# Performance work log

Measured on AMD Instinct MI355X. Metric: run time of the kernel, lower is better.

Reference implementation:

```python
import jax, jax.numpy as jnp
import numpy as np

E = 256; H = 8; HD = E // H
L_LEN = 300; A_LEN = 250
T = 768; B = 4
NEG = -1e9


def setup_inputs() -> dict:
    rng = jax.random.key(0)
    ks = jax.random.split(rng, 16)
    n = lambda k, s, sc=1.0: jax.random.normal(k, s, dtype=jnp.float32) * sc
    return {
        "query": n(ks[0], (T, B, E)),
        "key": n(ks[1], (T, B, E)),
        "value": n(ks[2], (T, B, E)),
        "in_proj_w": n(ks[3], (3 * E, E), 0.05),
        "in_proj_b": jnp.zeros((3 * E,), jnp.float32),
        "out_w": n(ks[4], (7, E, E), 0.05),
        "out_b": jnp.zeros((7, E), jnp.float32),
        "s_l_w": n(ks[5], (E, 4 * E), 0.05),
        "s_l_b": jnp.zeros((E,), jnp.float32),
        "s_a_w": n(ks[6], (E, 4 * E), 0.05),
        "s_a_b": jnp.zeros((E,), jnp.float32),
        "s_v_w": n(ks[7], (E, 4 * E), 0.05),
        "s_v_b": jnp.zeros((E,), jnp.float32),
        "final_w": n(ks[8], (E, E), 0.05),
        "final_b": jnp.zeros((E,), jnp.float32),
    }


def _forward(query, key, value, in_proj_w, in_proj_b, out_w, out_b,
             s_l_w, s_l_b, s_a_w, s_a_b, s_v_w, s_v_b, final_w, final_b):
    t, b, e = query.shape
    scaling = HD ** -0.5
    Wq, Wk, Wv = in_proj_w[:E], in_proj_w[E:2 * E], in_proj_w[2 * E:]
    bq, bk, bv = in_proj_b[:E], in_proj_b[E:2 * E], in_proj_b[2 * E:]
    q = (query @ Wq.T + bq) * scaling
    k = key @ Wk.T + bk
    v = value @ Wv.T + bv
    # (T, B, E) -> (B*H, T, HD)
    sh = lambda x: x.reshape(t, b * H, HD).transpose(1, 0, 2)
    q, k, v = sh(q), sh(k), sh(v)
    # shared QK^T, reused by all 7 masked branches
    scores = jnp.einsum('bth,bsh->bts', q, k)  # (B*H, T, T)
    idx = jnp.arange(t)
    seg = jnp.where(idx < L_LEN, 0, jnp.where(idx < L_LEN + A_LEN, 1, 2))

    def branch(i, mods):
        # m[j] = 1 iff position j belongs to one of the selected modalities
        m = sum((seg == s) for s in mods).astype(scores.dtype)  # (T,)
        # additive mask: in-set query attends only in-set keys; out-of-set
        # query rows get all -1e9 (uniform softmax, zeroed by row mask below)
        add = jnp.where((m[:, None] * m[None, :]) > 0, 0.0, NEG)
        w = jax.nn.softmax(scores + add, axis=-1) * m[None, :, None]
        o = jnp.einsum('bts,bsh->bth', w, v * m[None, :, None])
        o = o.transpose(1, 0, 2).reshape(t, b, e)
        return o @ out_w[i].T + out_b[i]

    attn_lav = branch(0, (0, 1, 2))
    attn_la = branch(1, (0, 1))
    attn_lv = branch(2, (0, 2))
    attn_av = branch(3, (1, 2))
    attn_l = branch(4, (0,))
    attn_a = branch(5, (1,))
    attn_v = branch(6, (2,))

    sl = jnp.concatenate([attn_lav, attn_la, attn_lv, attn_l], -1) @ s_l_w.T + s_l_b
    sa = jnp.concatenate([attn_lav, attn_la, attn_av, attn_a], -1) @ s_a_w.T + s_a_b
    sv = jnp.concatenate([attn_lav, attn_lv, attn_av, attn_v], -1) @ s_v_w.T + s_v_b
    return (sl + sa + sv) @ final_w.T + final_b


def reference(query, key, value, in_proj_w, in_proj_b, out_w, out_b,
              s_l_w, s_l_b, s_a_w, s_a_b, s_v_w, s_v_b, final_w, final_b):
    return _forward(query, key, value, in_proj_w, in_proj_b, out_w, out_b,
                    s_l_w, s_l_b, s_a_w, s_a_b, s_v_w, s_v_b, final_w, final_b)
```

## Files before the change

### kernel.cpp

```cpp
#include <hip/hip_runtime.h>
#include <hip/hip_bf16.h>

#define E 256
#define H 8
#define HD 32
#define T 768
#define B 4
#define BH 32

typedef __attribute__((ext_vector_type(8))) short bf16x8;
typedef __attribute__((ext_vector_type(4))) float f32x4;
typedef __attribute__((ext_vector_type(16))) float f32x16;

__device__ __forceinline__ float b2f(__hip_bfloat16 x) { return __bfloat162float(x); }

__device__ __forceinline__ unsigned short f2bf_u(float x) {
    __hip_bfloat16 h = __float2bfloat16(x);
    return *(unsigned short*)&h;
}
__device__ __forceinline__ float bfu2f(unsigned short u) {
    return __uint_as_float(((unsigned int)u) << 16);
}

__device__ __forceinline__ int detect_f32(const void* query) {
    const unsigned short* q = (const unsigned short*)query;
    int lane = threadIdx.x & 63;
    int bad = 0;
    #pragma unroll
    for (int i = 0; i < 4; ++i) {
        float v = bfu2f(q[lane + i * 64]);
        bad |= (!(v == v) || fabsf(v) > 1e4f) ? 1 : 0;
    }
    return __any(bad) ? 1 : 0;
}

__device__ __forceinline__ void f8_split(const float* v, bf16x8& h, bf16x8& l) {
    #pragma unroll
    for (int e = 0; e < 8; ++e) {
        unsigned short hu = f2bf_u(v[e]);
        h[e] = (short)hu;
        l[e] = (short)f2bf_u(v[e] - bfu2f(hu));
    }
}

#define MFMA3(ACC, AH, AL, BH_, BL_)                                         \
    ACC = __builtin_amdgcn_mfma_f32_16x16x32_bf16(AH, BH_, ACC, 0, 0, 0);    \
    ACC = __builtin_amdgcn_mfma_f32_16x16x32_bf16(AH, BL_, ACC, 0, 0, 0);    \
    ACC = __builtin_amdgcn_mfma_f32_16x16x32_bf16(AL, BH_, ACC, 0, 0, 0);

#define MFMA3W(ACC, AH, AL, BH_, BL_)                                        \
    ACC = __builtin_amdgcn_mfma_f32_32x32x16_bf16(AH, BH_, ACC, 0, 0, 0);    \
    ACC = __builtin_amdgcn_mfma_f32_32x32x16_bf16(AH, BL_, ACC, 0, 0, 0);    \
    ACC = __builtin_amdgcn_mfma_f32_32x32x16_bf16(AL, BH_, ACC, 0, 0, 0);

__device__ __forceinline__ bf16x8 mk8(int a, int b, int c, int d) {
    union { int i[4]; bf16x8 v; } u;
    u.i[0] = a; u.i[1] = b; u.i[2] = c; u.i[3] = d;
    return u.v;
}

__device__ __forceinline__ float ldu(const void* p, size_t i, int f32) {
    if (f32) return ((const float*)p)[i];
    return b2f(((const __hip_bfloat16*)p)[i]);
}

__device__ __forceinline__ float gsum_load(int i, int r2, int r,
                                           const void* sl, const void* sa,
                                           const void* sv, int f32)
{
    size_t base = (size_t)r2 * 1024;
    switch (i) {
        case 0: return ldu(sl, base + r, f32) + ldu(sa, base + r, f32) + ldu(sv, base + r, f32);
        case 1: return ldu(sl, base + 256 + r, f32) + ldu(sa, base + 256 + r, f32);
        case 2: return ldu(sl, base + 512 + r, f32) + ldu(sv, base + 256 + r, f32);
        case 3: return ldu(sa, base + 512 + r, f32) + ldu(sv, base + 512 + r, f32);
        case 4: return ldu(sl, base + 768 + r, f32);
        case 5: return ldu(sa, base + 768 + r, f32);
        default: return ldu(sv, base + 768 + r, f32);
    }
}

__global__ __launch_bounds__(256) void conv_kernel(
    const void* query, const void* key, const void* value, const void* w,
    const void* sl, const void* sa, const void* sv, const void* outw,
    unsigned short* __restrict__ XFh, unsigned short* __restrict__ XFl,
    unsigned short* __restrict__ WFh, unsigned short* __restrict__ WFl,
    unsigned short* __restrict__ GFh, unsigned short* __restrict__ GFl,
    unsigned short* __restrict__ OWFh, unsigned short* __restrict__ OWFl)
{
    int f32 = detect_f32(query);
    int item = blockIdx.x * 256 + threadIdx.x;
    if (item < 294912) {
        int inp = item / 98304;
        int rem = item % 98304;
        int row = rem >> 5, kg = rem & 31;
        const void* X = (inp == 0) ? query : (inp == 1) ? key : value;
        float v[8];
        if (f32) {
            const float4* p = (const float4*)((const float*)X +
                               (size_t)row * 256 + kg * 8);
            *(float4*)&v[0] = p[0];
            *(float4*)&v[4] = p[1];
        } else {
            #pragma unroll
            for (int j = 0; j < 8; ++j)
                v[j] = ldu(X, (size_t)row * 256 + kg * 8 + j, 0);
        }
        bf16x8 h, l;
        f8_split(v, h, l);
        int rb = row >> 4, kb = kg >> 2;
        int lane = (row & 15) | ((kg & 3) << 4);
        size_t idx = (((size_t)(inp * 192 + rb) * 8 + kb) * 64 + lane) * 8;
        *(bf16x8*)&XFh[idx] = h;
        *(bf16x8*)&XFl[idx] = l;
    } else if (item < 319488) {
        int rem = item - 294912;
        int gc = rem >> 5, kg = rem & 31;
        float v[8];
        if (f32) {
            const float4* p = (const float4*)((const float*)w +
                               (size_t)gc * 256 + kg * 8);
            *(float4*)&v[0] = p[0];
            *(float4*)&v[4] = p[1];
        } else {
            #pragma unroll
            for (int j = 0; j < 8; ++j)
                v[j] = ldu(w, (size_t)gc * 256 + kg * 8 + j, 0);
        }
        bf16x8 h, l;
        f8_split(v, h, l);
        int sec = gc >> 8, c = gc & 255;
        int cb = c >> 4, kb = kg >> 2;
        int lane = (c & 15) | ((kg & 3) << 4);
        size_t idx = (((size_t)(sec * 16 + cb) * 8 + kb) * 64 + lane) * 8;
        *(bf16x8*)&WFh[idx] = h;
        *(bf16x8*)&WFl[idx] = l;
    } else if (item < 376832) {
        int rem = item - 319488;
        int i = rem >> 13;
        int rest = rem & 8191;
        int r2 = rest >> 5, kg = rest & 31;
        float v[8];
        #pragma unroll
        for (int j = 0; j < 8; ++j)
            v[j] = gsum_load(i, r2, kg * 8 + j, sl, sa, sv, f32);
        bf16x8 h, l;
        f8_split(v, h, l);
        int rb = r2 >> 4, kb = kg >> 2;
        int lane = (r2 & 15) | ((kg & 3) << 4);
        size_t idx = (((size_t)(i * 16 + rb) * 8 + kb) * 64 + lane) * 8;
        *(bf16x8*)&GFh[idx] = h;
        *(bf16x8*)&GFl[idx] = l;
    } else if (item < 434176) {
        int rem = item - 376832;
        int i = rem >> 13;
        int rest = rem & 8191;
        int kg = rest >> 8, c = rest & 255;
        float v[8];
        #pragma unroll
        for (int j = 0; j < 8; ++j)
            v[j] = ldu(outw, (size_t)i * 65536 + (kg * 8 + j) * 256 + c, f32);
        bf16x8 h, l;
        f8_split(v, h, l);
        int cb = c >> 4, kb = kg >> 2;
        int lane = (c & 15) | ((kg & 3) << 4);
        size_t idx = (((size_t)(i * 16 + cb) * 8 + kb) * 64 + lane) * 8;
        *(bf16x8*)&OWFh[idx] = h;
        *(bf16x8*)&OWFl[idx] = l;
    }
}

__global__ __launch_bounds__(256) void qkv_mfma_kernel(
    const unsigned short* __restrict__ XFh, const unsigned short* __restrict__ XFl,
    const unsigned short* __restrict__ WFh, const unsigned short* __restrict__ WFl,
    const void* bias, const void* query,
    float* __restrict__ qws,
    unsigned short* __restrict__ KRh, unsigned short* __restrict__ KRl,
    unsigned short* __restrict__ VFh, unsigned short* __restrict__ VFl)
{
    int f32 = detect_f32(query);
    int bx = blockIdx.x;
    int rb = blockIdx.y;
    int sec = bx >> 2, cg = bx & 3;
    int w = threadIdx.x >> 6, lane = threadIdx.x & 63;
    int m = lane & 15, quad = lane >> 4;
    int cb = cg * 4 + w;

    const unsigned short* Ah = XFh + (((size_t)(sec * 192 + rb) * 8) * 64 + lane) * 8;
    const unsigned short* Al = XFl + (((size_t)(sec * 192 + rb) * 8) * 64 + lane) * 8;
    const unsigned short* Bh = WFh + (((size_t)(sec * 16 + cb) * 8) * 64 + lane) * 8;
    const unsigned short* Bl = WFl + (((size_t)(sec * 16 + cb) * 8) * 64 + lane) * 8;

    f32x4 acc = {};
    #pragma unroll
    for (int kb = 0; kb < 8; ++kb) {
        size_t off = (size_t)kb * 512;
        bf16x8 ah = *(const bf16x8*)(Ah + off);
        bf16x8 al = *(const bf16x8*)(Al + off);
        bf16x8 bh = *(const bf16x8*)(Bh + off);
        bf16x8 bl = *(const bf16x8*)(Bl + off);
        MFMA3(acc, ah, al, bh, bl)
    }

    int c_local = cb * 16 + m;
    float bv = ldu(bias, sec * 256 + c_local, f32);
    int h = c_local >> 5, hd = c_local & 31;

    if (sec == 0) {
        #pragma unroll
        for (int rr = 0; rr < 4; ++rr) {
            int row = rb * 16 + quad * 4 + rr;
            int t = row >> 2, b = row & 3;
            float val = (acc[rr] + bv) * 0.17677669529663687f;
            qws[((size_t)((b * H + h) * T + t)) * HD + hd] = val;
        }
    } else if (sec == 1) {
        #pragma unroll
        for (int rr = 0; rr < 4; ++rr) {
            int row = rb * 16 + quad * 4 + rr;
            int s = row >> 2, b = row & 3;
            int bh_ = b * 8 + h;
            float val = acc[rr] + bv;
            unsigned short hu = f2bf_u(val);
            unsigned short lu = f2bf_u(val - bfu2f(hu));
            size_t bi = ((size_t)bh_ * 768 + s) * 32 + hd;
            KRh[bi] = hu;
            KRl[bi] = lu;
        }
    } else {
        #pragma unroll
        for (int rr = 0; rr < 4; ++rr) {
            int row = rb * 16 + quad * 4 + rr;
            int s = row >> 2, b = row & 3;
            int bh_ = b * 8 + h;
            float val = acc[rr] + bv;
            unsigned short hu = f2bf_u(val);
            unsigned short lu = f2bf_u(val - bfu2f(hu));
            int s16 = s >> 4, hp = (s >> 3) & 1, j = s & 7;
            size_t bi = (((size_t)bh_ * 48 + s16) * 64 + hp * 32 + hd) * 8 + j;
            VFh[bi] = hu;
            VFl[bi] = lu;
        }
    }
}

__global__ __launch_bounds__(256) void wcomb1_mfma_kernel(
    const unsigned short* __restrict__ GFh, const unsigned short* __restrict__ GFl,
    const unsigned short* __restrict__ OWFh, const unsigned short* __restrict__ OWFl,
    float* __restrict__ Mtmp)
{
    int cgrp = blockIdx.x;
    int rb   = blockIdx.y;
    int i    = blockIdx.z;
    int w = threadIdx.x >> 6, lane = threadIdx.x & 63;
    int m = lane & 15, quad = lane >> 4;
    int cb = cgrp * 4 + w;

    const unsigned short* Ah = GFh + (((size_t)(i * 16 + rb) * 8) * 64 + lane) * 8;
    const unsigned short* Al = GFl + (((size_t)(i * 16 + rb) * 8) * 64 + lane) * 8;
    const unsigned short* Bh = OWFh + (((size_t)(i * 16 + cb) * 8) * 64 + lane) * 8;
    const unsigned short* Bl = OWFl + (((size_t)(i * 16 + cb) * 8) * 64 + lane) * 8;

    f32x4 acc = {};
    #pragma unroll
    for (int kb = 0; kb < 8; ++kb) {
        size_t off = (size_t)kb * 512;
        bf16x8 ah = *(const bf16x8*)(Ah + off);
        bf16x8 al = *(const bf16x8*)(Al + off);
        bf16x8 bh = *(const bf16x8*)(Bh + off);
        bf16x8 bl = *(const bf16x8*)(Bl + off);
        MFMA3(acc, ah, al, bh, bl)
    }
    #pragma unroll
    for (int rr = 0; rr < 4; ++rr) {
        int r2 = rb * 16 + quad * 4 + rr;
        Mtmp[(size_t)i * 65536 + r2 * 256 + cb * 16 + m] = acc[rr];
    }
}

__global__ __launch_bounds__(256, 3) void attn_mfma_kernel(
    const float* __restrict__ qws,
    const unsigned short* __restrict__ KRh, const unsigned short* __restrict__ KRl,
    const unsigned short* __restrict__ VFh, const unsigned short* __restrict__ VFl,
    unsigned short* __restrict__ Ohi, unsigned short* __restrict__ Olo)
{
    int tile = blockIdx.x;
    int bh   = blockIdx.y;
    int t0 = tile * 32;
    int tid = threadIdx.x;
    int w = tid >> 6, lane = tid & 63;
    int ln = lane & 31, h = lane >> 5;

    __shared__ float AC2[2][3][32][36];
    __shared__ float SS2[2][3][32];

    bf16x8 qbh[2], qbl[2];
    {
        const float* qr = qws + ((size_t)bh * T + t0 + ln) * HD + h * 8;
        #pragma unroll
        for (int c = 0; c < 2; ++c) {
            float qv[8];
            *(float4*)&qv[0] = *(const float4*)(qr + c * 16);
            *(float4*)&qv[4] = *(const float4*)(qr + c * 16 + 4);
            f8_split(qv, qbh[c], qbl[c]);
        }
    }

    f32x16 accA = {}, accB = {};
    float ssA = 0.f, ssB = 0.f;

    for (int q = 0; q < 3; ++q) {
        int ch = w * 3 + q;
        int sbase = ch * 64;
        int route = (ch == 5) ? 1 : (ch == 4 || ch == 8) ? 2 : 0;
        int bnd = (ch == 4) ? 300 : 550;
        bool c12 = (ch == 4);

        int PH[2][8], PL[2][8];
        #pragma unroll
        for (int st = 0; st < 2; ++st) {
            size_t krow = ((size_t)bh * 768 + sbase + st * 32 + ln) * 32 + h * 8;
            bf16x8 kh0 = *(const bf16x8*)(KRh + krow);
            bf16x8 kl0 = *(const bf16x8*)(KRl + krow);
            bf16x8 kh1 = *(const bf16x8*)(KRh + krow + 16);
            bf16x8 kl1 = *(const bf16x8*)(KRl + krow + 16);
            f32x16 d = {};
            MFMA3W(d, kh0, kl0, qbh[0], qbl[0])
            MFMA3W(d, kh1, kl1, qbh[1], qbl[1])

            int EH[16], EL[16];
            #pragma unroll
            for (int r = 0; r < 16; ++r) {
                float e = __expf(d[r]);
                if (route == 2) {
                    int s = sbase + st * 32 + (r & 3) + 8 * (r >> 2) + 4 * h;
                    if (s < bnd) ssA += e; else ssB += e;
                } else if (route == 1) ssB += e;
                else ssA += e;
                unsigned int eb = __float_as_uint(e);
                float lo = e - __uint_as_float(eb & 0xffff0000u);
                EH[r] = (int)eb;
                EL[r] = (int)__float_as_uint(lo);
            }
            #pragma unroll
            for (int p = 0; p < 8; ++p) {
                PH[st][p] = (int)(((unsigned)EH[2*p] >> 16) |
                                  ((unsigned)EH[2*p+1] & 0xffff0000u));
                PL[st][p] = (int)(((unsigned)EL[2*p] >> 16) |
                                  ((unsigned)EL[2*p+1] & 0xffff0000u));
            }
        }

        #pragma unroll
        for (int ks = 0; ks < 4; ++ks) {
            int st = ks >> 1, cc = 4 * (ks & 1);
            size_t vidx = (((size_t)bh * 48 + ch * 4 + ks) * 64 + lane) * 8;
            bf16x8 vbh = *(const bf16x8*)(VFh + vidx);
            bf16x8 vbl = *(const bf16x8*)(VFl + vidx);

            int sh0 = __shfl_xor(PH[st][cc+0], 32);
            int sh1 = __shfl_xor(PH[st][cc+1], 32);
            int sh2 = __shfl_xor(PH[st][cc+2], 32);
            int sh3 = __shfl_xor(PH[st][cc+3], 32);
            int sl0 = __shfl_xor(PL[st][cc+0], 32);
            int sl1 = __shfl_xor(PL[st][cc+1], 32);
            int sl2 = __shfl_xor(PL[st][cc+2], 32);
            int sl3 = __shfl_xor(PL[st][cc+3], 32);
            int FH0 = h ? sh2 : PH[st][cc+0];
            int FH1 = h ? sh3 : PH[st][cc+1];
            int FH2 = h ? PH[st][cc+2] : sh0;
            int FH3 = h ? PH[st][cc+3] : sh1;
            int FL0 = h ? sl2 : PL[st][cc+0];
            int FL1 = h ? sl3 : PL[st][cc+1];
            int FL2 = h ? PL[st][cc+2] : sl0;
            int FL3 = h ? PL[st][cc+3] : sl1;
            bf16x8 feh = mk8(FH0, FH1, FH2, FH3);
            bf16x8 fel = mk8(FL0, FL1, FL2, FL3);

            if (route == 0)      { MFMA3W(accA, feh, fel, vbh, vbl) }
            else if (route == 1) { MFMA3W(accB, feh, fel, vbh, vbl) }
            else {
                if (ks < 2)       { MFMA3W(accA, feh, fel, vbh, vbl) }
                else if (ks == 3) { MFMA3W(accB, feh, fel, vbh, vbl) }
                else {
                    int a0 = h ? (c12 ? FH0 : 0) : FH0;
                    int a1 = h ? (c12 ? FH1 : 0) : FH1;
                    int a2 = h ? 0 : FH2;
                    int a3 = h ? 0 : (c12 ? FH3 : 0);
                    int b0 = h ? (c12 ? 0 : FH0) : 0;
                    int b1 = h ? (c12 ? 0 : FH1) : 0;
                    int b2 = h ? FH2 : 0;
                    int b3 = h ? FH3 : (c12 ? 0 : FH3);
                    int la0 = h ? (c12 ? FL0 : 0) : FL0;
                    int la1 = h ? (c12 ? FL1 : 0) : FL1;
                    int la2 = h ? 0 : FL2;
                    int la3 = h ? 0 : (c12 ? FL3 : 0);
                    int lb0 = h ? (c12 ? 0 : FL0) : 0;
                    int lb1 = h ? (c12 ? 0 : FL1) : 0;
                    int lb2 = h ? FL2 : 0;
                    int lb3 = h ? FL3 : (c12 ? 0 : FL3);
                    bf16x8 fha = mk8(a0, a1, a2, a3), fla = mk8(la0, la1, la2, la3);
                    bf16x8 fhb = mk8(b0, b1, b2, b3), flb = mk8(lb0, lb1, lb2, lb3);
                    MFMA3W(accA, fha, fla, vbh, vbl)
                    MFMA3W(accB, fhb, flb, vbh, vbl)
                }
            }
        }
    }

    ssA += __shfl_xor(ssA, 32);
    ssB += __shfl_xor(ssB, 32);

    int bsel = w & 1;
    f32x16 zz = {};
    f32x16 o0 = (w <= 1) ? accA : zz;
    f32x16 o1 = (w == 1) ? accB : (w == 2) ? accA : zz;
    f32x16 o2 = (w == 2) ? accB : (w == 3) ? accA : zz;
    float s0 = (w <= 1) ? ssA : 0.f;
    float s1 = (w == 1) ? ssB : (w == 2) ? ssA : 0.f;
    float s2 = (w == 2) ? ssB : (w == 3) ? ssA : 0.f;

    if (w < 2) {
        #pragma unroll
        for (int r = 0; r < 16; ++r) {
            int t = (r & 3) + 8 * (r >> 2) + 4 * h;
            AC2[bsel][0][t][ln] = o0[r];
            AC2[bsel][1][t][ln] = o1[r];
            AC2[bsel][2][t][ln] = o2[r];
        }
        if (h == 0) {
            SS2[bsel][0][ln] = s0;
            SS2[bsel][1][ln] = s1;
            SS2[bsel][2][ln] = s2;
        }
    }
    __syncthreads();
    if (w >= 2) {
        #pragma unroll
        for (int r = 0; r < 16; ++r) {
            int t = (r & 3) + 8 * (r >> 2) + 4 * h;
            AC2[bsel][1][t][ln] += o1[r];
            AC2[bsel][2][t][ln] += o2[r];
        }
        if (h == 0) {
            SS2[bsel][1][ln] += s1;
            SS2[bsel][2][ln] += s2;
        }
    }
    __syncthreads();

    int tt = tid >> 3, q4 = tid & 7;
    float Pv[3][4], S[3];
    #pragma unroll
    for (int sg = 0; sg < 3; ++sg) {
        const float4 a = *(const float4*)&AC2[0][sg][tt][q4 * 4];
        const float4 b = *(const float4*)&AC2[1][sg][tt][q4 * 4];
        Pv[sg][0] = a.x + b.x; Pv[sg][1] = a.y + b.y;
        Pv[sg][2] = a.z + b.z; Pv[sg][3] = a.w + b.w;
        S[sg] = SS2[0][sg][tt] + SS2[1][sg][tt];
    }

    int t_glob = t0 + tt;
    int g = (t_glob < 300) ? 0 : (t_glob < 550 ? 1 : 2);
    int b_ = bh >> 3, h_ = bh & 7;
    int row = t_glob * B + b_;
    int lslot = (row & 15) + ((q4 >> 1) << 4);
    int j0 = (q4 & 1) * 4;
    size_t fbase = (((size_t)(row >> 4) * 56 + h_) * 64 + lslot) * 8 + j0;
    const int masks[7] = {7, 3, 5, 6, 1, 2, 4};
    #pragma unroll
    for (int i = 0; i < 7; ++i) {
        int mm = masks[i];
        float n0 = 0.f, n1 = 0.f, n2 = 0.f, n3 = 0.f, den = 0.f;
        if (mm & 1) { n0 += Pv[0][0]; n1 += Pv[0][1]; n2 += Pv[0][2]; n3 += Pv[0][3]; den += S[0]; }
        if (mm & 2) { n0 += Pv[1][0]; n1 += Pv[1][1]; n2 += Pv[1][2]; n3 += Pv[1][3]; den += S[1]; }
        if (mm & 4) { n0 += Pv[2][0]; n1 += Pv[2][1]; n2 += Pv[2][2]; n3 += Pv[2][3]; den += S[2]; }
        float r = 1.f / den;
        int live = (mm >> g) & 1;
        float o[4];
        o[0] = live ? n0 * r : 0.f;
        o[1] = live ? n1 * r : 0.f;
        o[2] = live ? n2 * r : 0.f;
        o[3] = live ? n3 * r : 0.f;
        ushort4 hi4, lo4;
        unsigned short* hp = (unsigned short*)&hi4;
        unsigned short* lp = (unsigned short*)&lo4;
        #pragma unroll
        for (int j = 0; j < 4; ++j) {
            unsigned short hu = f2bf_u(o[j]);
            hp[j] = hu;
            lp[j] = f2bf_u(o[j] - bfu2f(hu));
        }
        size_t addr = fbase + (size_t)i * (8 * 64 * 8);
        *(ushort4*)&Ohi[addr] = hi4;
        *(ushort4*)&Olo[addr] = lo4;
    }
}

__global__ __launch_bounds__(256) void wcomb2_gemm_kernel(
    const float* __restrict__ Mtmp, const void* finalw, const void* query,
    unsigned short* __restrict__ DThi, unsigned short* __restrict__ DTlo)
{
    int f32 = detect_f32(query);
    int bx = blockIdx.x;
    int by = blockIdx.y;
    int i  = blockIdx.z;
    int tid = threadIdx.x;
    int tx = tid & 15, ty = tid >> 4;
    int colbase = bx * 32, rowbase = by * 32;
    __shared__ __align__(16) float AsT[32][34];
    __shared__ __align__(16) float Bs[32][34];
    float acc[2][2] = {};

    for (int kb = 0; kb < 8; ++kb) {
        __syncthreads();
        #pragma unroll
        for (int l = 0; l < 4; ++l) {
            int idx = l * 256 + tid;
            int c = idx & 31, kk = idx >> 5;
            AsT[kk][c] = Mtmp[(size_t)i * 65536 + (kb * 32 + kk) * 256 + rowbase + c];
            int k2 = idx & 31, n = idx >> 5;
            Bs[k2][n] = ldu(finalw, (size_t)(colbase + n) * 256 + kb * 32 + k2, f32);
        }
        __syncthreads();
        #pragma unroll 8
        for (int kk = 0; kk < 32; ++kk) {
            const float2 av = *(const float2*)&AsT[kk][ty * 2];
            const float2 bv = *(const float2*)&Bs[kk][tx * 2];
            acc[0][0] += av.x * bv.x; acc[0][1] += av.x * bv.y;
            acc[1][0] += av.y * bv.x; acc[1][1] += av.y * bv.y;
        }
    }
    #pragma unroll
    for (int u = 0; u < 2; ++u)
        #pragma unroll
        for (int v = 0; v < 2; ++v) {
            int c = rowbase + ty * 2 + u, e = colbase + tx * 2 + v;
            float a = acc[u][v];
            unsigned short hu = f2bf_u(a);
            size_t fidx = (((size_t)(e >> 4) * 56 + i * 8 + (c >> 5)) * 64
                           + (e & 15) + (((c >> 3) & 3) << 4)) * 8 + (c & 7);
            DThi[fidx] = hu;
            DTlo[fidx] = f2bf_u(a - bfu2f(hu));
        }
}

__global__ __launch_bounds__(256) void bias1_kernel(
    const void* sl, const void* sa, const void* sv, const void* outb,
    const void* slb, const void* sab, const void* svb,
    const void* query, float* __restrict__ c0)
{
    int f32 = detect_f32(query);
    int r2 = blockIdx.x, m = threadIdx.x;
    __shared__ float red[256];
    float acc = 0.f;
    #pragma unroll
    for (int i = 0; i < 7; ++i)
        acc += ldu(outb, i * 256 + m, f32) * gsum_load(i, r2, m, sl, sa, sv, f32);
    red[m] = acc;
    __syncthreads();
    for (int s = 128; s > 0; s >>= 1) {
        if (m < s) red[m] += red[m + s];
        __syncthreads();
    }
    if (m == 0)
        c0[r2] = red[0] + ldu(slb, r2, f32) + ldu(sab, r2, f32) + ldu(svb, r2, f32);
}

__global__ __launch_bounds__(256) void bias2_kernel(
    const float* __restrict__ c0, const void* finalw, const void* finalb,
    const void* query, float* __restrict__ d0)
{
    int f32 = detect_f32(query);
    int e = blockIdx.x, r = threadIdx.x;
    __shared__ float red[256];
    red[r] = c0[r] * ldu(finalw, (size_t)e * 256 + r, f32);
    __syncthreads();
    for (int s = 128; s > 0; s >>= 1) {
        if (r < s) red[r] += red[r + s];
        __syncthreads();
    }
    if (r == 0)
        d0[e] = red[0] + ldu(finalb, e, f32);
}

__global__ __launch_bounds__(256) void final_gemm_mfma_kernel(
    const unsigned short* __restrict__ Ohi, const unsigned short* __restrict__ Olo,
    const unsigned short* __restrict__ DThi, const unsigned short* __restrict__ DTlo,
    const float* __restrict__ d0, const void* query,
    void* __restrict__ outv)
{
    int f32 = detect_f32(query);
    int bx = blockIdx.x;
    int by = blockIdx.y;
    int w  = threadIdx.x >> 6;
    int lane = threadIdx.x & 63;
    int m = lane & 15, quad = lane >> 4;
    int R0 = by * 16, C0 = bx * 64 + w * 16;

    int t0 = R0 >> 2, t1 = (R0 + 15) >> 2;
    int g0 = (t0 < 300) ? 0 : (t0 < 550 ? 1 : 2);
    int g1 = (t1 < 300) ? 0 : (t1 < 550 ? 1 : 2);
    int activeset = (1 << g0) | (1 << g1);
    const int masks[7] = {7, 3, 5, 6, 1, 2, 4};

    const unsigned short* Abase_h = Ohi + (size_t)by * 56 * 512 + lane * 8;
    const unsigned short* Abase_l = Olo + (size_t)by * 56 * 512 + lane * 8;
    const unsigned short* Bbase_h = DThi + (size_t)(bx * 4 + w) * 56 * 512 + lane * 8;
    const unsigned short* Bbase_l = DTlo + (size_t)(bx * 4 + w) * 56 * 512 + lane * 8;

    f32x4 acc = {};
    for (int i = 0; i < 7; ++i) {
        if (!(masks[i] & activeset)) continue;
        #pragma unroll
        for (int kb = 0; kb < 8; ++kb) {
            size_t off = (size_t)(i * 8 + kb) * 512;
            bf16x8 ah = *(const bf16x8*)(Abase_h + off);
            bf16x8 al = *(const bf16x8*)(Abase_l + off);
            bf16x8 bh = *(const bf16x8*)(Bbase_h + off);
            bf16x8 bl = *(const bf16x8*)(Bbase_l + off);
            acc = __builtin_amdgcn_mfma_f32_16x16x32_bf16(ah, bh, acc, 0, 0, 0);
            acc = __builtin_amdgcn_mfma_f32_16x16x32_bf16(ah, bl, acc, 0, 0, 0);
            acc = __builtin_amdgcn_mfma_f32_16x16x32_bf16(al, bh, acc, 0, 0, 0);
        }
    }
    float dv = d0[C0 + m];
    #pragma unroll
    for (int r = 0; r < 4; ++r) {
        int row = R0 + quad * 4 + r;
        int col = C0 + m;
        float val = acc[r] + dv;
        if (f32) ((float*)outv)[(size_t)row * 256 + col] = val;
        else ((__hip_bfloat16*)outv)[(size_t)row * 256 + col] = __float2bfloat16(val);
    }
}

extern "C" void kernel_launch(void* const* d_in, const int* in_sizes, int n_in,
                              void* d_out, int out_size, void* d_ws, size_t ws_size,
                              hipStream_t stream) {
    const void* query     = d_in[0];
    const void* key       = d_in[1];
    const void* value     = d_in[2];
    const void* in_proj_w = d_in[3];
    const void* in_proj_b = d_in[4];
    const void* out_w     = d_in[5];
    const void* out_b     = d_in[6];
    const void* s_l_w     = d_in[7];
    const void* s_l_b     = d_in[8];
    const void* s_a_w     = d_in[9];
    const void* s_a_b     = d_in[10];
    const void* s_v_w     = d_in[11];
    const void* s_v_b     = d_in[12];
    const void* final_w   = d_in[13];
    const void* final_b   = d_in[14];

    float* ws     = (float*)d_ws;
    float* qws    = ws;
    unsigned short* KRh = (unsigned short*)(ws + 786432);
    unsigned short* KRl = KRh + 786432;
    unsigned short* VFh = (unsigned short*)(ws + 1572864);
    unsigned short* VFl = VFh + 786432;
    unsigned short* Ohi = (unsigned short*)(ws + 2359296);
    unsigned short* Olo = (unsigned short*)(ws + 5111808);
    unsigned short* XFh = (unsigned short*)(ws + 2359296);
    unsigned short* XFl = XFh + 2359296;
    unsigned short* WFh = XFl + 2359296;
    unsigned short* WFl = WFh + 196608;
    unsigned short* GFh = (unsigned short*)(ws + 4915200);
    unsigned short* GFl = GFh + 458752;
    unsigned short* OWFh = GFl + 458752;
    unsigned short* OWFl = OWFh + 458752;
    float* Mtmp   = ws + 7864320;
    unsigned short* DThi = (unsigned short*)(ws + 8323072);
    unsigned short* DTlo = (unsigned short*)(ws + 8552448);
    float* d0     = ws + 8781824;
    float* c0     = Mtmp;

    conv_kernel<<<1696, 256, 0, stream>>>(query, key, value, in_proj_w,
                                          s_l_w, s_a_w, s_v_w, out_w,
                                          XFh, XFl, WFh, WFl,
                                          GFh, GFl, OWFh, OWFl);
    qkv_mfma_kernel<<<dim3(12, 192), 256, 0, stream>>>(XFh, XFl, WFh, WFl,
                                                       in_proj_b, query, qws,
                                                       KRh, KRl, VFh, VFl);
    wcomb1_mfma_kernel<<<dim3(4, 16, 7), 256, 0, stream>>>(GFh, GFl, OWFh, OWFl,
                                                           Mtmp);
    attn_mfma_kernel<<<dim3(24, 32), 256, 0, stream>>>(qws, KRh, KRl, VFh, VFl,
                                                       Ohi, Olo);
    wcomb2_gemm_kernel<<<dim3(8, 8, 7), 256, 0, stream>>>(Mtmp, final_w, query,
                                                          DThi, DTlo);
    bias1_kernel<<<256, 256, 0, stream>>>(s_l_w, s_a_w, s_v_w, out_b,
                                          s_l_b, s_a_b, s_v_b, query, c0);
    bias2_kernel<<<256, 256, 0, stream>>>(c0, final_w, final_b, query, d0);
    final_gemm_mfma_kernel<<<dim3(4, 192), 256, 0, stream>>>(Ohi, Olo, DThi, DTlo,
                                                             d0, query, d_out);
}
```

Measured before the change: 183.3 us.

## Merge independent kernels into three staged launches to cut launch count

Folds the eight kernel launches into four by packing independent work into shared grids. Bias1 joins the conversion kernel, QKV projection plus wcomb1 plus bias2 form one launch, and attention plus wcomb2 form another, with roles picked by block index ranges. This removes launch gaps and lets the smaller independent pieces fill idle CUs alongside the large ones. In exchange, merged kernels share the largest register and LDS footprint and the attention launch bounds. c0 moves to its own buffer so it no longer aliases Mtmp.

```diff
diff --git a/kernel.cpp b/kernel.cpp
--- a/kernel.cpp
+++ b/kernel.cpp
@@ -80,508 +80,503 @@
     }
 }
 
-__global__ __launch_bounds__(256) void conv_kernel(
+__global__ __launch_bounds__(256) void stage1_kernel(
     const void* query, const void* key, const void* value, const void* w,
     const void* sl, const void* sa, const void* sv, const void* outw,
+    const void* outb, const void* slb, const void* sab, const void* svb,
     unsigned short* __restrict__ XFh, unsigned short* __restrict__ XFl,
     unsigned short* __restrict__ WFh, unsigned short* __restrict__ WFl,
     unsigned short* __restrict__ GFh, unsigned short* __restrict__ GFl,
-    unsigned short* __restrict__ OWFh, unsigned short* __restrict__ OWFl)
+    unsigned short* __restrict__ OWFh, unsigned short* __restrict__ OWFl,
+    float* __restrict__ c0)
 {
+    __shared__ float red[256];
     int f32 = detect_f32(query);
-    int item = blockIdx.x * 256 + threadIdx.x;
-    if (item < 294912) {
-        int inp = item / 98304;
-        int rem = item % 98304;
-        int row = rem >> 5, kg = rem & 31;
-        const void* X = (inp == 0) ? query : (inp == 1) ? key : value;
-        float v[8];
-        if (f32) {
-            const float4* p = (const float4*)((const float*)X +
-                               (size_t)row * 256 + kg * 8);
-            *(float4*)&v[0] = p[0];
-            *(float4*)&v[4] = p[1];
-        } else {
+    if (blockIdx.x < 1696) {
+        int item = blockIdx.x * 256 + threadIdx.x;
+        if (item < 294912) {
+            int inp = item / 98304;
+            int rem = item % 98304;
+            int row = rem >> 5, kg = rem & 31;
+            const void* X = (inp == 0) ? query : (inp == 1) ? key : value;
+            float v[8];
+            if (f32) {
+                const float4* p = (const float4*)((const float*)X +
+                                   (size_t)row * 256 + kg * 8);
+                *(float4*)&v[0] = p[0];
+                *(float4*)&v[4] = p[1];
+            } else {
+                #pragma unroll
+                for (int j = 0; j < 8; ++j)
+                    v[j] = ldu(X, (size_t)row * 256 + kg * 8 + j, 0);
+            }
+            bf16x8 h, l;
+            f8_split(v, h, l);
+            int rb = row >> 4, kb = kg >> 2;
+            int lane = (row & 15) | ((kg & 3) << 4);
+            size_t idx = (((size_t)(inp * 192 + rb) * 8 + kb) * 64 + lane) * 8;
+            *(bf16x8*)&XFh[idx] = h;
+            *(bf16x8*)&XFl[idx] = l;
+        } else if (item < 319488) {
+            int rem = item - 294912;
+            int gc = rem >> 5, kg = rem & 31;
+            float v[8];
+            if (f32) {
+                const float4* p = (const float4*)((const float*)w +
+                                   (size_t)gc * 256 + kg * 8);
+                *(float4*)&v[0] = p[0];
+                *(float4*)&v[4] = p[1];
+            } else {
+                #pragma unroll
+                for (int j = 0; j < 8; ++j)
+                    v[j] = ldu(w, (size_t)gc * 256 + kg * 8 + j, 0);
+            }
+            bf16x8 h, l;
+            f8_split(v, h, l);
+            int sec = gc >> 8, c = gc & 255;
+            int cb = c >> 4, kb = kg >> 2;
+            int lane = (c & 15) | ((kg & 3) << 4);
+            size_t idx = (((size_t)(sec * 16 + cb) * 8 + kb) * 64 + lane) * 8;
+            *(bf16x8*)&WFh[idx] = h;
+            *(bf16x8*)&WFl[idx] = l;
+        } else if (item < 376832) {
+            int rem = item - 319488;
+            int i = rem >> 13;
+            int rest = rem & 8191;
+            int r2 = rest >> 5, kg = rest & 31;
+            float v[8];
             #pragma unroll
             for (int j = 0; j < 8; ++j)
-                v[j] = ldu(X, (size_t)row * 256 + kg * 8 + j, 0);
-        }
-        bf16x8 h, l;
-        f8_split(v, h, l);
-        int rb = row >> 4, kb = kg >> 2;
-        int lane = (row & 15) | ((kg & 3) << 4);
-        size_t idx = (((size_t)(inp * 192 + rb) * 8 + kb) * 64 + lane) * 8;
-        *(bf16x8*)&XFh[idx] = h;
-        *(bf16x8*)&XFl[idx] = l;
-    } else if (item < 319488) {
-        int rem = item - 294912;
-        int gc = rem >> 5, kg = rem & 31;
-        float v[8];
-        if (f32) {
-            const float4* p = (const float4*)((const float*)w +
-                               (size_t)gc * 256 + kg * 8);
-            *(float4*)&v[0] = p[0];
-            *(float4*)&v[4] = p[1];
-        } else {
+                v[j] = gsum_load(i, r2, kg * 8 + j, sl, sa, sv, f32);
+            bf16x8 h, l;
+            f8_split(v, h, l);
+            int rb = r2 >> 4, kb = kg >> 2;
+            int lane = (r2 & 15) | ((kg & 3) << 4);
+            size_t idx = (((size_t)(i * 16 + rb) * 8 + kb) * 64 + lane) * 8;
+            *(bf16x8*)&GFh[idx] = h;
+            *(bf16x8*)&GFl[idx] = l;
+        } else if (item < 434176) {
+            int rem = item - 376832;
+            int i = rem >> 13;
+            int rest = rem & 8191;
+            int kg = rest >> 8, c = rest & 255;
+            float v[8];
             #pragma unroll
             for (int j = 0; j < 8; ++j)
-                v[j] = ldu(w, (size_t)gc * 256 + kg * 8 + j, 0);
-        }
-        bf16x8 h, l;
-        f8_split(v, h, l);
-        int sec = gc >> 8, c = gc & 255;
-        int cb = c >> 4, kb = kg >> 2;
-        int lane = (c & 15) | ((kg & 3) << 4);
-        size_t idx = (((size_t)(sec * 16 + cb) * 8 + kb) * 64 + lane) * 8;
-        *(bf16x8*)&WFh[idx] = h;
-        *(bf16x8*)&WFl[idx] = l;
-    } else if (item < 376832) {
-        int rem = item - 319488;
-        int i = rem >> 13;
-        int rest = rem & 8191;
-        int r2 = rest >> 5, kg = rest & 31;
-        float v[8];
-        #pragma unroll
-        for (int j = 0; j < 8; ++j)
-            v[j] = gsum_load(i, r2, kg * 8 + j, sl, sa, sv, f32);
-        bf16x8 h, l;
-        f8_split(v, h, l);
-        int rb = r2 >> 4, kb = kg >> 2;
-        int lane = (r2 & 15) | ((kg & 3) << 4);
-        size_t idx = (((size_t)(i * 16 + rb) * 8 + kb) * 64 + lane) * 8;
-        *(bf16x8*)&GFh[idx] = h;
-        *(bf16x8*)&GFl[idx] = l;
-    } else if (item < 434176) {
-        int rem = item - 376832;
-        int i = rem >> 13;
-        int rest = rem & 8191;
-        int kg = rest >> 8, c = rest & 255;
-        float v[8];
-        #pragma unroll
-        for (int j = 0; j < 8; ++j)
-            v[j] = ldu(outw, (size_t)i * 65536 + (kg * 8 + j) * 256 + c, f32);
-        bf16x8 h, l;
-        f8_split(v, h, l);
-        int cb = c >> 4, kb = kg >> 2;
-        int lane = (c & 15) | ((kg & 3) << 4);
-        size_t idx = (((size_t)(i * 16 + cb) * 8 + kb) * 64 + lane) * 8;
-        *(bf16x8*)&OWFh[idx] = h;
-        *(bf16x8*)&OWFl[idx] = l;
-    }
-}
-
-__global__ __launch_bounds__(256) void qkv_mfma_kernel(
+                v[j] = ldu(outw, (size_t)i * 65536 + (kg * 8 + j) * 256 + c, f32);
+            bf16x8 h, l;
+            f8_split(v, h, l);
+            int cb = c >> 4, kb = kg >> 2;
+            int lane = (c & 15) | ((kg & 3) << 4);
+            size_t idx = (((size_t)(i * 16 + cb) * 8 + kb) * 64 + lane) * 8;
+            *(bf16x8*)&OWFh[idx] = h;
+            *(bf16x8*)&OWFl[idx] = l;
+        }
+    } else {
+        int r2 = blockIdx.x - 1696, m = threadIdx.x;
+        float acc = 0.f;
+        #pragma unroll
+        for (int i = 0; i < 7; ++i)
+            acc += ldu(outb, i * 256 + m, f32) * gsum_load(i, r2, m, sl, sa, sv, f32);
+        red[m] = acc;
+        __syncthreads();
+        for (int s = 128; s > 0; s >>= 1) {
+            if (m < s) red[m] += red[m + s];
+            __syncthreads();
+        }
+        if (m == 0)
+            c0[r2] = red[0] + ldu(slb, r2, f32) + ldu(sab, r2, f32) + ldu(svb, r2, f32);
+    }
+}
+
+__global__ __launch_bounds__(256) void stage2_kernel(
     const unsigned short* __restrict__ XFh, const unsigned short* __restrict__ XFl,
     const unsigned short* __restrict__ WFh, const unsigned short* __restrict__ WFl,
     const void* bias, const void* query,
     float* __restrict__ qws,
     unsigned short* __restrict__ KRh, unsigned short* __restrict__ KRl,
-    unsigned short* __restrict__ VFh, unsigned short* __restrict__ VFl)
-{
-    int f32 = detect_f32(query);
-    int bx = blockIdx.x;
-    int rb = blockIdx.y;
-    int sec = bx >> 2, cg = bx & 3;
-    int w = threadIdx.x >> 6, lane = threadIdx.x & 63;
-    int m = lane & 15, quad = lane >> 4;
-    int cb = cg * 4 + w;
-
-    const unsigned short* Ah = XFh + (((size_t)(sec * 192 + rb) * 8) * 64 + lane) * 8;
-    const unsigned short* Al = XFl + (((size_t)(sec * 192 + rb) * 8) * 64 + lane) * 8;
-    const unsigned short* Bh = WFh + (((size_t)(sec * 16 + cb) * 8) * 64 + lane) * 8;
-    const unsigned short* Bl = WFl + (((size_t)(sec * 16 + cb) * 8) * 64 + lane) * 8;
-
-    f32x4 acc = {};
-    #pragma unroll
-    for (int kb = 0; kb < 8; ++kb) {
-        size_t off = (size_t)kb * 512;
-        bf16x8 ah = *(const bf16x8*)(Ah + off);
-        bf16x8 al = *(const bf16x8*)(Al + off);
-        bf16x8 bh = *(const bf16x8*)(Bh + off);
-        bf16x8 bl = *(const bf16x8*)(Bl + off);
-        MFMA3(acc, ah, al, bh, bl)
-    }
-
-    int c_local = cb * 16 + m;
-    float bv = ldu(bias, sec * 256 + c_local, f32);
-    int h = c_local >> 5, hd = c_local & 31;
-
-    if (sec == 0) {
-        #pragma unroll
-        for (int rr = 0; rr < 4; ++rr) {
-            int row = rb * 16 + quad * 4 + rr;
-            int t = row >> 2, b = row & 3;
-            float val = (acc[rr] + bv) * 0.17677669529663687f;
-            qws[((size_t)((b * H + h) * T + t)) * HD + hd] = val;
-        }
-    } else if (sec == 1) {
-        #pragma unroll
-        for (int rr = 0; rr < 4; ++rr) {
-            int row = rb * 16 + quad * 4 + rr;
-            int s = row >> 2, b = row & 3;
-            int bh_ = b * 8 + h;
-            float val = acc[rr] + bv;
-            unsigned short hu = f2bf_u(val);
-            unsigned short lu = f2bf_u(val - bfu2f(hu));
-            size_t bi = ((size_t)bh_ * 768 + s) * 32 + hd;
-            KRh[bi] = hu;
-            KRl[bi] = lu;
-        }
-    } else {
-        #pragma unroll
-        for (int rr = 0; rr < 4; ++rr) {
-            int row = rb * 16 + quad * 4 + rr;
-            int s = row >> 2, b = row & 3;
-            int bh_ = b * 8 + h;
-            float val = acc[rr] + bv;
-            unsigned short hu = f2bf_u(val);
-            unsigned short lu = f2bf_u(val - bfu2f(hu));
-            int s16 = s >> 4, hp = (s >> 3) & 1, j = s & 7;
-            size_t bi = (((size_t)bh_ * 48 + s16) * 64 + hp * 32 + hd) * 8 + j;
-            VFh[bi] = hu;
-            VFl[bi] = lu;
-        }
-    }
-}
-
-__global__ __launch_bounds__(256) void wcomb1_mfma_kernel(
+    unsigned short* __restrict__ VFh, unsigned short* __restrict__ VFl,
     const unsigned short* __restrict__ GFh, const unsigned short* __restrict__ GFl,
     const unsigned short* __restrict__ OWFh, const unsigned short* __restrict__ OWFl,
-    float* __restrict__ Mtmp)
+    float* __restrict__ Mtmp,
+    const float* __restrict__ c0, const void* finalw, const void* finalb,
+    float* __restrict__ d0)
 {
-    int cgrp = blockIdx.x;
-    int rb   = blockIdx.y;
-    int i    = blockIdx.z;
-    int w = threadIdx.x >> 6, lane = threadIdx.x & 63;
-    int m = lane & 15, quad = lane >> 4;
-    int cb = cgrp * 4 + w;
-
-    const unsigned short* Ah = GFh + (((size_t)(i * 16 + rb) * 8) * 64 + lane) * 8;
-    const unsigned short* Al = GFl + (((size_t)(i * 16 + rb) * 8) * 64 + lane) * 8;
-    const unsigned short* Bh = OWFh + (((size_t)(i * 16 + cb) * 8) * 64 + lane) * 8;
-    const unsigned short* Bl = OWFl + (((size_t)(i * 16 + cb) * 8) * 64 + lane) * 8;
-
-    f32x4 acc = {};
-    #pragma unroll
-    for (int kb = 0; kb < 8; ++kb) {
-        size_t off = (size_t)kb * 512;
-        bf16x8 ah = *(const bf16x8*)(Ah + off);
-        bf16x8 al = *(const bf16x8*)(Al + off);
-        bf16x8 bh = *(const bf16x8*)(Bh + off);
-        bf16x8 bl = *(const bf16x8*)(Bl + off);
-        MFMA3(acc, ah, al, bh, bl)
-    }
-    #pragma unroll
-    for (int rr = 0; rr < 4; ++rr) {
-        int r2 = rb * 16 + quad * 4 + rr;
-        Mtmp[(size_t)i * 65536 + r2 * 256 + cb * 16 + m] = acc[rr];
-    }
-}
-
-__global__ __launch_bounds__(256, 3) void attn_mfma_kernel(
+    __shared__ float red[256];
+    int bxx = blockIdx.x;
+    if (bxx < 2304) {
+        int f32 = detect_f32(query);
+        int bx = bxx % 12;
+        int rb = bxx / 12;
+        int sec = bx >> 2, cg = bx & 3;
+        int w = threadIdx.x >> 6, lane = threadIdx.x & 63;
+        int m = lane & 15, quad = lane >> 4;
+        int cb = cg * 4 + w;
+
+        const unsigned short* Ah = XFh + (((size_t)(sec * 192 + rb) * 8) * 64 + lane) * 8;
+        const unsigned short* Al = XFl + (((size_t)(sec * 192 + rb) * 8) * 64 + lane) * 8;
+        const unsigned short* Bh = WFh + (((size_t)(sec * 16 + cb) * 8) * 64 + lane) * 8;
+        const unsigned short* Bl = WFl + (((size_t)(sec * 16 + cb) * 8) * 64 + lane) * 8;
+
+        f32x4 acc = {};
+        #pragma unroll
+        for (int kb = 0; kb < 8; ++kb) {
+            size_t off = (size_t)kb * 512;
+            bf16x8 ah = *(const bf16x8*)(Ah + off);
+            bf16x8 al = *(const bf16x8*)(Al + off);
+            bf16x8 bh = *(const bf16x8*)(Bh + off);
+            bf16x8 bl = *(const bf16x8*)(Bl + off);
+            MFMA3(acc, ah, al, bh, bl)
+        }
+
+        int c_local = cb * 16 + m;
+        float bv = ldu(bias, sec * 256 + c_local, f32);
+        int h = c_local >> 5, hd = c_local & 31;
+
+        if (sec == 0) {
+            #pragma unroll
+            for (int rr = 0; rr < 4; ++rr) {
+                int row = rb * 16 + quad * 4 + rr;
+                int t = row >> 2, b = row & 3;
+                float val = (acc[rr] + bv) * 0.17677669529663687f;
+                qws[((size_t)((b * H + h) * T + t)) * HD + hd] = val;
+            }
+        } else if (sec == 1) {
+            #pragma unroll
+            for (int rr = 0; rr < 4; ++rr) {
+                int row = rb * 16 + quad * 4 + rr;
+                int s = row >> 2, b = row & 3;
+                int bh_ = b * 8 + h;
+                float val = acc[rr] + bv;
+                unsigned short hu = f2bf_u(val);
+                unsigned short lu = f2bf_u(val - bfu2f(hu));
+                size_t bi = ((size_t)bh_ * 768 + s) * 32 + hd;
+                KRh[bi] = hu;
+                KRl[bi] = lu;
+            }
+        } else {
+            #pragma unroll
+            for (int rr = 0; rr < 4; ++rr) {
+                int row = rb * 16 + quad * 4 + rr;
+                int s = row >> 2, b = row & 3;
+                int bh_ = b * 8 + h;
+                float val = acc[rr] + bv;
+                unsigned short hu = f2bf_u(val);
+                unsigned short lu = f2bf_u(val - bfu2f(hu));
+                int s16 = s >> 4, hp = (s >> 3) & 1, j = s & 7;
+                size_t bi = (((size_t)bh_ * 48 + s16) * 64 + hp * 32 + hd) * 8 + j;
+                VFh[bi] = hu;
+                VFl[bi] = lu;
+            }
+        }
+    } else if (bxx < 2752) {
+        int idx = bxx - 2304;
+        int cgrp = idx & 3;
+        int rb   = (idx >> 2) & 15;
+        int i    = idx >> 6;
+        int w = threadIdx.x >> 6, lane = threadIdx.x & 63;
+        int m = lane & 15, quad = lane >> 4;
+        int cb = cgrp * 4 + w;
+
+        const unsigned short* Ah = GFh + (((size_t)(i * 16 + rb) * 8) * 64 + lane) * 8;
+        const unsigned short* Al = GFl + (((size_t)(i * 16 + rb) * 8) * 64 + lane) * 8;
+        const unsigned short* Bh = OWFh + (((size_t)(i * 16 + cb) * 8) * 64 + lane) * 8;
+        const unsigned short* Bl = OWFl + (((size_t)(i * 16 + cb) * 8) * 64 + lane) * 8;
+
+        f32x4 acc = {};
+        #pragma unroll
+        for (int kb = 0; kb < 8; ++kb) {
+            size_t off = (size_t)kb * 512;
+            bf16x8 ah = *(const bf16x8*)(Ah + off);
+            bf16x8 al = *(const bf16x8*)(Al + off);
+            bf16x8 bh = *(const bf16x8*)(Bh + off);
+            bf16x8 bl = *(const bf16x8*)(Bl + off);
+            MFMA3(acc, ah, al, bh, bl)
+        }
+        #pragma unroll
+        for (int rr = 0; rr < 4; ++rr) {
+            int r2 = rb * 16 + quad * 4 + rr;
+            Mtmp[(size_t)i * 65536 + r2 * 256 + cb * 16 + m] = acc[rr];
+        }
+    } else {
+        int f32 = detect_f32(query);
+        int e = bxx - 2752, r = threadIdx.x;
+        red[r] = c0[r] * ldu(finalw, (size_t)e * 256 + r, f32);
+        __syncthreads();
+        for (int s = 128; s > 0; s >>= 1) {
+            if (r < s) red[r] += red[r + s];
+            __syncthreads();
+        }
+        if (r == 0)
+            d0[e] = red[0] + ldu(finalb, e, f32);
+    }
+}
+
+__global__ __launch_bounds__(256, 3) void stage3_kernel(
     const float* __restrict__ qws,
     const unsigned short* __restrict__ KRh, const unsigned short* __restrict__ KRl,
     const unsigned short* __restrict__ VFh, const unsigned short* __restrict__ VFl,
-    unsigned short* __restrict__ Ohi, unsigned short* __restrict__ Olo)
-{
-    int tile = blockIdx.x;
-    int bh   = blockIdx.y;
-    int t0 = tile * 32;
-    int tid = threadIdx.x;
-    int w = tid >> 6, lane = tid & 63;
-    int ln = lane & 31, h = lane >> 5;
-
-    __shared__ float AC2[2][3][32][36];
-    __shared__ float SS2[2][3][32];
-
-    bf16x8 qbh[2], qbl[2];
-    {
-        const float* qr = qws + ((size_t)bh * T + t0 + ln) * HD + h * 8;
-        #pragma unroll
-        for (int c = 0; c < 2; ++c) {
-            float qv[8];
-            *(float4*)&qv[0] = *(const float4*)(qr + c * 16);
-            *(float4*)&qv[4] = *(const float4*)(qr + c * 16 + 4);
-            f8_split(qv, qbh[c], qbl[c]);
-        }
-    }
-
-    f32x16 accA = {}, accB = {};
-    float ssA = 0.f, ssB = 0.f;
-
-    for (int q = 0; q < 3; ++q) {
-        int ch = w * 3 + q;
-        int sbase = ch * 64;
-        int route = (ch == 5) ? 1 : (ch == 4 || ch == 8) ? 2 : 0;
-        int bnd = (ch == 4) ? 300 : 550;
-        bool c12 = (ch == 4);
-
-        int PH[2][8], PL[2][8];
-        #pragma unroll
-        for (int st = 0; st < 2; ++st) {
-            size_t krow = ((size_t)bh * 768 + sbase + st * 32 + ln) * 32 + h * 8;
-            bf16x8 kh0 = *(const bf16x8*)(KRh + krow);
-            bf16x8 kl0 = *(const bf16x8*)(KRl + krow);
-            bf16x8 kh1 = *(const bf16x8*)(KRh + krow + 16);
-            bf16x8 kl1 = *(const bf16x8*)(KRl + krow + 16);
-            f32x16 d = {};
-            MFMA3W(d, kh0, kl0, qbh[0], qbl[0])
-            MFMA3W(d, kh1, kl1, qbh[1], qbl[1])
-
-            int EH[16], EL[16];
-            #pragma unroll
-            for (int r = 0; r < 16; ++r) {
-                float e = __expf(d[r]);
-                if (route == 2) {
-                    int s = sbase + st * 32 + (r & 3) + 8 * (r >> 2) + 4 * h;
-                    if (s < bnd) ssA += e; else ssB += e;
-                } else if (route == 1) ssB += e;
-                else ssA += e;
-                unsigned int eb = __float_as_uint(e);
-                float lo = e - __uint_as_float(eb & 0xffff0000u);
-                EH[r] = (int)eb;
-                EL[r] = (int)__float_as_uint(lo);
-            }
-            #pragma unroll
-            for (int p = 0; p < 8; ++p) {
-                PH[st][p] = (int)(((unsigned)EH[2*p] >> 16) |
-                                  ((unsigned)EH[2*p+1] & 0xffff0000u));
-                PL[st][p] = (int)(((unsigned)EL[2*p] >> 16) |
-                                  ((unsigned)EL[2*p+1] & 0xffff0000u));
-            }
-        }
-
-        #pragma unroll
-        for (int ks = 0; ks < 4; ++ks) {
-            int st = ks >> 1, cc = 4 * (ks & 1);
-            size_t vidx = (((size_t)bh * 48 + ch * 4 + ks) * 64 + lane) * 8;
-            bf16x8 vbh = *(const bf16x8*)(VFh + vidx);
-            bf16x8 vbl = *(const bf16x8*)(VFl + vidx);
-
-            int sh0 = __shfl_xor(PH[st][cc+0], 32);
-            int sh1 = __shfl_xor(PH[st][cc+1], 32);
-            int sh2 = __shfl_xor(PH[st][cc+2], 32);
-            int sh3 = __shfl_xor(PH[st][cc+3], 32);
-            int sl0 = __shfl_xor(PL[st][cc+0], 32);
-            int sl1 = __shfl_xor(PL[st][cc+1], 32);
-            int sl2 = __shfl_xor(PL[st][cc+2], 32);
-            int sl3 = __shfl_xor(PL[st][cc+3], 32);
-            int FH0 = h ? sh2 : PH[st][cc+0];
-            int FH1 = h ? sh3 : PH[st][cc+1];
-            int FH2 = h ? PH[st][cc+2] : sh0;
-            int FH3 = h ? PH[st][cc+3] : sh1;
-            int FL0 = h ? sl2 : PL[st][cc+0];
-            int FL1 = h ? sl3 : PL[st][cc+1];
-            int FL2 = h ? PL[st][cc+2] : sl0;
-            int FL3 = h ? PL[st][cc+3] : sl1;
-            bf16x8 feh = mk8(FH0, FH1, FH2, FH3);
-            bf16x8 fel = mk8(FL0, FL1, FL2, FL3);
-
-            if (route == 0)      { MFMA3W(accA, feh, fel, vbh, vbl) }
-            else if (route == 1) { MFMA3W(accB, feh, fel, vbh, vbl) }
-            else {
-                if (ks < 2)       { MFMA3W(accA, feh, fel, vbh, vbl) }
-                else if (ks == 3) { MFMA3W(accB, feh, fel, vbh, vbl) }
-                else {
-                    int a0 = h ? (c12 ? FH0 : 0) : FH0;
-                    int a1 = h ? (c12 ? FH1 : 0) : FH1;
-                    int a2 = h ? 0 : FH2;
-                    int a3 = h ? 0 : (c12 ? FH3 : 0);
-                    int b0 = h ? (c12 ? 0 : FH0) : 0;
-                    int b1 = h ? (c12 ? 0 : FH1) : 0;
-                    int b2 = h ? FH2 : 0;
-                    int b3 = h ? FH3 : (c12 ? 0 : FH3);
-                    int la0 = h ? (c12 ? FL0 : 0) : FL0;
-                    int la1 = h ? (c12 ? FL1 : 0) : FL1;
-                    int la2 = h ? 0 : FL2;
-                    int la3 = h ? 0 : (c12 ? FL3 : 0);
-                    int lb0 = h ? (c12 ? 0 : FL0) : 0;
-                    int lb1 = h ? (c12 ? 0 : FL1) : 0;
-                    int lb2 = h ? FL2 : 0;
-                    int lb3 = h ? FL3 : (c12 ? 0 : FL3);
-                    bf16x8 fha = mk8(a0, a1, a2, a3), fla = mk8(la0, la1, la2, la3);
-                    bf16x8 fhb = mk8(b0, b1, b2, b3), flb = mk8(lb0, lb1, lb2, lb3);
-                    MFMA3W(accA, fha, fla, vbh, vbl)
-                    MFMA3W(accB, fhb, flb, vbh, vbl)
-                }
-            }
-        }
-    }
-
-    ssA += __shfl_xor(ssA, 32);
-    ssB += __shfl_xor(ssB, 32);
-
-    int bsel = w & 1;
-    f32x16 zz = {};
-    f32x16 o0 = (w <= 1) ? accA : zz;
-    f32x16 o1 = (w == 1) ? accB : (w == 2) ? accA : zz;
-    f32x16 o2 = (w == 2) ? accB : (w == 3) ? accA : zz;
-    float s0 = (w <= 1) ? ssA : 0.f;
-    float s1 = (w == 1) ? ssB : (w == 2) ? ssA : 0.f;
-    float s2 = (w == 2) ? ssB : (w == 3) ? ssA : 0.f;
-
-    if (w < 2) {
-        #pragma unroll
-        for (int r = 0; r < 16; ++r) {
-            int t = (r & 3) + 8 * (r >> 2) + 4 * h;
-            AC2[bsel][0][t][ln] = o0[r];
-            AC2[bsel][1][t][ln] = o1[r];
-            AC2[bsel][2][t][ln] = o2[r];
-        }
-        if (h == 0) {
-            SS2[bsel][0][ln] = s0;
-            SS2[bsel][1][ln] = s1;
-            SS2[bsel][2][ln] = s2;
-        }
-    }
-    __syncthreads();
-    if (w >= 2) {
-        #pragma unroll
-        for (int r = 0; r < 16; ++r) {
-            int t = (r & 3) + 8 * (r >> 2) + 4 * h;
-            AC2[bsel][1][t][ln] += o1[r];
-            AC2[bsel][2][t][ln] += o2[r];
-        }
-        if (h == 0) {
-            SS2[bsel][1][ln] += s1;
-            SS2[bsel][2][ln] += s2;
-        }
-    }
-    __syncthreads();
-
-    int tt = tid >> 3, q4 = tid & 7;
-    float Pv[3][4], S[3];
-    #pragma unroll
-    for (int sg = 0; sg < 3; ++sg) {
-        const float4 a = *(const float4*)&AC2[0][sg][tt][q4 * 4];
-        const float4 b = *(const float4*)&AC2[1][sg][tt][q4 * 4];
-        Pv[sg][0] = a.x + b.x; Pv[sg][1] = a.y + b.y;
-        Pv[sg][2] = a.z + b.z; Pv[sg][3] = a.w + b.w;
-        S[sg] = SS2[0][sg][tt] + SS2[1][sg][tt];
-    }
-
-    int t_glob = t0 + tt;
-    int g = (t_glob < 300) ? 0 : (t_glob < 550 ? 1 : 2);
-    int b_ = bh >> 3, h_ = bh & 7;
-    int row = t_glob * B + b_;
-    int lslot = (row & 15) + ((q4 >> 1) << 4);
-    int j0 = (q4 & 1) * 4;
-    size_t fbase = (((size_t)(row >> 4) * 56 + h_) * 64 + lslot) * 8 + j0;
-    const int masks[7] = {7, 3, 5, 6, 1, 2, 4};
-    #pragma unroll
-    for (int i = 0; i < 7; ++i) {
-        int mm = masks[i];
-        float n0 = 0.f, n1 = 0.f, n2 = 0.f, n3 = 0.f, den = 0.f;
-        if (mm & 1) { n0 += Pv[0][0]; n1 += Pv[0][1]; n2 += Pv[0][2]; n3 += Pv[0][3]; den += S[0]; }
-        if (mm & 2) { n0 += Pv[1][0]; n1 += Pv[1][1]; n2 += Pv[1][2]; n3 += Pv[1][3]; den += S[1]; }
-        if (mm & 4) { n0 += Pv[2][0]; n1 += Pv[2][1]; n2 += Pv[2][2]; n3 += Pv[2][3]; den += S[2]; }
-        float r = 1.f / den;
-        int live = (mm >> g) & 1;
-        float o[4];
-        o[0] = live ? n0 * r : 0.f;
-        o[1] = live ? n1 * r : 0.f;
-        o[2] = live ? n2 * r : 0.f;
-        o[3] = live ? n3 * r : 0.f;
-        ushort4 hi4, lo4;
-        unsigned short* hp = (unsigned short*)&hi4;
-        unsigned short* lp = (unsigned short*)&lo4;
-        #pragma unroll
-        for (int j = 0; j < 4; ++j) {
-            unsigned short hu = f2bf_u(o[j]);
-            hp[j] = hu;
-            lp[j] = f2bf_u(o[j] - bfu2f(hu));
-        }
-        size_t addr = fbase + (size_t)i * (8 * 64 * 8);
-        *(ushort4*)&Ohi[addr] = hi4;
-        *(ushort4*)&Olo[addr] = lo4;
-    }
-}
-
-__global__ __launch_bounds__(256) void wcomb2_gemm_kernel(
+    unsigned short* __restrict__ Ohi, unsigned short* __restrict__ Olo,
     const float* __restrict__ Mtmp, const void* finalw, const void* query,
     unsigned short* __restrict__ DThi, unsigned short* __restrict__ DTlo)
 {
-    int f32 = detect_f32(query);
-    int bx = blockIdx.x;
-    int by = blockIdx.y;
-    int i  = blockIdx.z;
+    __shared__ __align__(16) float SMEM[7104];
     int tid = threadIdx.x;
-    int tx = tid & 15, ty = tid >> 4;
-    int colbase = bx * 32, rowbase = by * 32;
-    __shared__ __align__(16) float AsT[32][34];
-    __shared__ __align__(16) float Bs[32][34];
-    float acc[2][2] = {};
-
-    for (int kb = 0; kb < 8; ++kb) {
+
+    if (blockIdx.x < 768) {
+        float (*AC2)[3][32][36] = (float(*)[3][32][36])&SMEM[0];
+        float (*SS2)[3][32]     = (float(*)[3][32])&SMEM[6912];
+        int tile = blockIdx.x % 24;
+        int bh   = blockIdx.x / 24;
+        int t0 = tile * 32;
+        int w = tid >> 6, lane = tid & 63;
+        int ln = lane & 31, h = lane >> 5;
+
+        bf16x8 qbh[2], qbl[2];
+        {
+            const float* qr = qws + ((size_t)bh * T + t0 + ln) * HD + h * 8;
+            #pragma unroll
+            for (int c = 0; c < 2; ++c) {
+                float qv[8];
+                *(float4*)&qv[0] = *(const float4*)(qr + c * 16);
+                *(float4*)&qv[4] = *(const float4*)(qr + c * 16 + 4);
+                f8_split(qv, qbh[c], qbl[c]);
+            }
+        }
+
+        f32x16 accA = {}, accB = {};
+        float ssA = 0.f, ssB = 0.f;
+
+        for (int q = 0; q < 3; ++q) {
+            int ch = w * 3 + q;
+            int sbase = ch * 64;
+            int route = (ch == 5) ? 1 : (ch == 4 || ch == 8) ? 2 : 0;
+            int bnd = (ch == 4) ? 300 : 550;
+            bool c12 = (ch == 4);
+
+            int PH[2][8], PL[2][8];
+            #pragma unroll
+            for (int st = 0; st < 2; ++st) {
+                size_t krow = ((size_t)bh * 768 + sbase + st * 32 + ln) * 32 + h * 8;
+                bf16x8 kh0 = *(const bf16x8*)(KRh + krow);
+                bf16x8 kl0 = *(const bf16x8*)(KRl + krow);
+                bf16x8 kh1 = *(const bf16x8*)(KRh + krow + 16);
+                bf16x8 kl1 = *(const bf16x8*)(KRl + krow + 16);
+                f32x16 d = {};
+                MFMA3W(d, kh0, kl0, qbh[0], qbl[0])
+                MFMA3W(d, kh1, kl1, qbh[1], qbl[1])
+
+                int EH[16], EL[16];
+                #pragma unroll
+                for (int r = 0; r < 16; ++r) {
+                    float e = __expf(d[r]);
+                    if (route == 2) {
+                        int s = sbase + st * 32 + (r & 3) + 8 * (r >> 2) + 4 * h;
+                        if (s < bnd) ssA += e; else ssB += e;
+                    } else if (route == 1) ssB += e;
+                    else ssA += e;
+                    unsigned int eb = __float_as_uint(e);
+                    float lo = e - __uint_as_float(eb & 0xffff0000u);
+                    EH[r] = (int)eb;
+                    EL[r] = (int)__float_as_uint(lo);
+                }
+                #pragma unroll
+                for (int p = 0; p < 8; ++p) {
+                    PH[st][p] = (int)(((unsigned)EH[2*p] >> 16) |
+                                      ((unsigned)EH[2*p+1] & 0xffff0000u));
+                    PL[st][p] = (int)(((unsigned)EL[2*p] >> 16) |
+                                      ((unsigned)EL[2*p+1] & 0xffff0000u));
+                }
+            }
+
+            #pragma unroll
+            for (int ks = 0; ks < 4; ++ks) {
+                int st = ks >> 1, cc = 4 * (ks & 1);
+                size_t vidx = (((size_t)bh * 48 + ch * 4 + ks) * 64 + lane) * 8;
+                bf16x8 vbh = *(const bf16x8*)(VFh + vidx);
+                bf16x8 vbl = *(const bf16x8*)(VFl + vidx);
+
+                int sh0 = __shfl_xor(PH[st][cc+0], 32);
+                int sh1 = __shfl_xor(PH[st][cc+1], 32);
+                int sh2 = __shfl_xor(PH[st][cc+2], 32);
+                int sh3 = __shfl_xor(PH[st][cc+3], 32);
+                int sl0 = __shfl_xor(PL[st][cc+0], 32);
+                int sl1 = __shfl_xor(PL[st][cc+1], 32);
+                int sl2 = __shfl_xor(PL[st][cc+2], 32);
+                int sl3 = __shfl_xor(PL[st][cc+3], 32);
+                int FH0 = h ? sh2 : PH[st][cc+0];
+                int FH1 = h ? sh3 : PH[st][cc+1];
+                int FH2 = h ? PH[st][cc+2] : sh0;
+                int FH3 = h ? PH[st][cc+3] : sh1;
+                int FL0 = h ? sl2 : PL[st][cc+0];
+                int FL1 = h ? sl3 : PL[st][cc+1];
+                int FL2 = h ? PL[st][cc+2] : sl0;
+                int FL3 = h ? PL[st][cc+3] : sl1;
+                bf16x8 feh = mk8(FH0, FH1, FH2, FH3);
+                bf16x8 fel = mk8(FL0, FL1, FL2, FL3);
+
+                if (route == 0)      { MFMA3W(accA, feh, fel, vbh, vbl) }
+                else if (route == 1) { MFMA3W(accB, feh, fel, vbh, vbl) }
+                else {
+                    if (ks < 2)       { MFMA3W(accA, feh, fel, vbh, vbl) }
+                    else if (ks == 3) { MFMA3W(accB, feh, fel, vbh, vbl) }
+                    else {
+                        int a0 = h ? (c12 ? FH0 : 0) : FH0;
+                        int a1 = h ? (c12 ? FH1 : 0) : FH1;
+                        int a2 = h ? 0 : FH2;
+                        int a3 = h ? 0 : (c12 ? FH3 : 0);
+                        int b0 = h ? (c12 ? 0 : FH0) : 0;
+                        int b1 = h ? (c12 ? 0 : FH1) : 0;
+                        int b2 = h ? FH2 : 0;
+                        int b3 = h ? FH3 : (c12 ? 0 : FH3);
+                        int la0 = h ? (c12 ? FL0 : 0) : FL0;
+                        int la1 = h ? (c12 ? FL1 : 0) : FL1;
+                        int la2 = h ? 0 : FL2;
+                        int la3 = h ? 0 : (c12 ? FL3 : 0);
+                        int lb0 = h ? (c12 ? 0 : FL0) : 0;
+                        int lb1 = h ? (c12 ? 0 : FL1) : 0;
+                        int lb2 = h ? FL2 : 0;
+                        int lb3 = h ? FL3 : (c12 ? 0 : FL3);
+                        bf16x8 fha = mk8(a0, a1, a2, a3), fla = mk8(la0, la1, la2, la3);
+                        bf16x8 fhb = mk8(b0, b1, b2, b3), flb = mk8(lb0, lb1, lb2, lb3);
+                        MFMA3W(accA, fha, fla, vbh, vbl)
+                        MFMA3W(accB, fhb, flb, vbh, vbl)
+                    }
+                }
+            }
+        }
+
+        ssA += __shfl_xor(ssA, 32);
+        ssB += __shfl_xor(ssB, 32);
+
+        int bsel = w & 1;
+        f32x16 zz = {};
+        f32x16 o0 = (w <= 1) ? accA : zz;
+        f32x16 o1 = (w == 1) ? accB : (w == 2) ? accA : zz;
+        f32x16 o2 = (w == 2) ? accB : (w == 3) ? accA : zz;
+        float s0 = (w <= 1) ? ssA : 0.f;
+        float s1 = (w == 1) ? ssB : (w == 2) ? ssA : 0.f;
+        float s2 = (w == 2) ? ssB : (w == 3) ? ssA : 0.f;
+
+        if (w < 2) {
+            #pragma unroll
+            for (int r = 0; r < 16; ++r) {
+                int t = (r & 3) + 8 * (r >> 2) + 4 * h;
+                AC2[bsel][0][t][ln] = o0[r];
+                AC2[bsel][1][t][ln] = o1[r];
+                AC2[bsel][2][t][ln] = o2[r];
+            }
+            if (h == 0) {
+                SS2[bsel][0][ln] = s0;
+                SS2[bsel][1][ln] = s1;
+                SS2[bsel][2][ln] = s2;
+            }
+        }
         __syncthreads();
-        #pragma unroll
-        for (int l = 0; l < 4; ++l) {
-            int idx = l * 256 + tid;
-            int c = idx & 31, kk = idx >> 5;
-            AsT[kk][c] = Mtmp[(size_t)i * 65536 + (kb * 32 + kk) * 256 + rowbase + c];
-            int k2 = idx & 31, n = idx >> 5;
-            Bs[k2][n] = ldu(finalw, (size_t)(colbase + n) * 256 + kb * 32 + k2, f32);
+        if (w >= 2) {
+            #pragma unroll
+            for (int r = 0; r < 16; ++r) {
+                int t = (r & 3) + 8 * (r >> 2) + 4 * h;
+                AC2[bsel][1][t][ln] += o1[r];
+                AC2[bsel][2][t][ln] += o2[r];
+            }
+            if (h == 0) {
+                SS2[bsel][1][ln] += s1;
+                SS2[bsel][2][ln] += s2;
+            }
         }
         __syncthreads();
-        #pragma unroll 8
-        for (int kk = 0; kk < 32; ++kk) {
-            const float2 av = *(const float2*)&AsT[kk][ty * 2];
-            const float2 bv = *(const float2*)&Bs[kk][tx * 2];
-            acc[0][0] += av.x * bv.x; acc[0][1] += av.x * bv.y;
-            acc[1][0] += av.y * bv.x; acc[1][1] += av.y * bv.y;
-        }
-    }
-    #pragma unroll
-    for (int u = 0; u < 2; ++u)
-        #pragma unroll
-        for (int v = 0; v < 2; ++v) {
-            int c = rowbase + ty * 2 + u, e = colbase + tx * 2 + v;
-            float a = acc[u][v];
-            unsigned short hu = f2bf_u(a);
-            size_t fidx = (((size_t)(e >> 4) * 56 + i * 8 + (c >> 5)) * 64
-                           + (e & 15) + (((c >> 3) & 3) << 4)) * 8 + (c & 7);
-            DThi[fidx] = hu;
-            DTlo[fidx] = f2bf_u(a - bfu2f(hu));
-        }
-}
-
-__global__ __launch_bounds__(256) void bias1_kernel(
-    const void* sl, const void* sa, const void* sv, const void* outb,
-    const void* slb, const void* sab, const void* svb,
-    const void* query, float* __restrict__ c0)
-{
-    int f32 = detect_f32(query);
-    int r2 = blockIdx.x, m = threadIdx.x;
-    __shared__ float red[256];
-    float acc = 0.f;
-    #pragma unroll
-    for (int i = 0; i < 7; ++i)
-        acc += ldu(outb, i * 256 + m, f32) * gsum_load(i, r2, m, sl, sa, sv, f32);
-    red[m] = acc;
-    __syncthreads();
-    for (int s = 128; s > 0; s >>= 1) {
-        if (m < s) red[m] += red[m + s];
-        __syncthreads();
-    }
-    if (m == 0)
-        c0[r2] = red[0] + ldu(slb, r2, f32) + ldu(sab, r2, f32) + ldu(svb, r2, f32);
-}
-
-__global__ __launch_bounds__(256) void bias2_kernel(
-    const float* __restrict__ c0, const void* finalw, const void* finalb,
-    const void* query, float* __restrict__ d0)
-{
-    int f32 = detect_f32(query);
-    int e = blockIdx.x, r = threadIdx.x;
-    __shared__ float red[256];
-    red[r] = c0[r] * ldu(finalw, (size_t)e * 256 + r, f32);
-    __syncthreads();
-    for (int s = 128; s > 0; s >>= 1) {
-        if (r < s) red[r] += red[r + s];
-        __syncthreads();
-    }
-    if (r == 0)
-        d0[e] = red[0] + ldu(finalb, e, f32);
+
+        int tt = tid >> 3, q4 = tid & 7;
+        float Pv[3][4], S[3];
+        #pragma unroll
+        for (int sg = 0; sg < 3; ++sg) {
+            const float4 a = *(const float4*)&AC2[0][sg][tt][q4 * 4];
+            const float4 b = *(const float4*)&AC2[1][sg][tt][q4 * 4];
+            Pv[sg][0] = a.x + b.x; Pv[sg][1] = a.y + b.y;
+            Pv[sg][2] = a.z + b.z; Pv[sg][3] = a.w + b.w;
+            S[sg] = SS2[0][sg][tt] + SS2[1][sg][tt];
+        }
+
+        int t_glob = t0 + tt;
+        int g = (t_glob < 300) ? 0 : (t_glob < 550 ? 1 : 2);
+        int b_ = bh >> 3, h_ = bh & 7;
+        int row = t_glob * B + b_;
+        int lslot = (row & 15) + ((q4 >> 1) << 4);
+        int j0 = (q4 & 1) * 4;
+        size_t fbase = (((size_t)(row >> 4) * 56 + h_) * 64 + lslot) * 8 + j0;
+        const int masks[7] = {7, 3, 5, 6, 1, 2, 4};
+        #pragma unroll
+        for (int i = 0; i < 7; ++i) {
+            int mm = masks[i];
+            float n0 = 0.f, n1 = 0.f, n2 = 0.f, n3 = 0.f, den = 0.f;
+            if (mm & 1) { n0 += Pv[0][0]; n1 += Pv[0][1]; n2 += Pv[0][2]; n3 += Pv[0][3]; den += S[0]; }
+            if (mm & 2) { n0 += Pv[1][0]; n1 += Pv[1][1]; n2 += Pv[1][2]; n3 += Pv[1][3]; den += S[1]; }
+            if (mm & 4) { n0 += Pv[2][0]; n1 += Pv[2][1]; n2 += Pv[2][2]; n3 += Pv[2][3]; den += S[2]; }
+            float r = 1.f / den;
+            int live = (mm >> g) & 1;
+            float o[4];
+            o[0] = live ? n0 * r : 0.f;
+            o[1] = live ? n1 * r : 0.f;
+            o[2] = live ? n2 * r : 0.f;
+            o[3] = live ? n3 * r : 0.f;
+            ushort4 hi4, lo4;
+            unsigned short* hp = (unsigned short*)&hi4;
+            unsigned short* lp = (unsigned short*)&lo4;
+            #pragma unroll
+            for (int j = 0; j < 4; ++j) {
+                unsigned short hu = f2bf_u(o[j]);
+                hp[j] = hu;
+                lp[j] = f2bf_u(o[j] - bfu2f(hu));
+            }
+            size_t addr = fbase + (size_t)i * (8 * 64 * 8);
+            *(ushort4*)&Ohi[addr] = hi4;
+            *(ushort4*)&Olo[addr] = lo4;
+        }
+    } else {
+        float (*AsT)[34] = (float(*)[34])&SMEM[0];
+        float (*Bs)[34]  = (float(*)[34])&SMEM[1088];
+        int f32 = detect_f32(query);
+        int idx = blockIdx.x - 768;
+        int bx = idx & 7;
+        int by = (idx >> 3) & 7;
+        int i  = idx >> 6;
+        int tx = tid & 15, ty = tid >> 4;
+        int colbase = bx * 32, rowbase = by * 32;
+        float acc[2][2] = {};
+
+        for (int kb = 0; kb < 8; ++kb) {
+            __syncthreads();
+            #pragma unroll
+            for (int l = 0; l < 4; ++l) {
+                int idx2 = l * 256 + tid;
+                int c = idx2 & 31, kk = idx2 >> 5;
+                AsT[kk][c] = Mtmp[(size_t)i * 65536 + (kb * 32 + kk) * 256 + rowbase + c];
+                int k2 = idx2 & 31, n = idx2 >> 5;
+                Bs[k2][n] = ldu(finalw, (size_t)(colbase + n) * 256 + kb * 32 + k2, f32);
+            }
+            __syncthreads();
+            #pragma unroll 8
+            for (int kk = 0; kk < 32; ++kk) {
+                const float2 av = *(const float2*)&AsT[kk][ty * 2];
+                const float2 bv = *(const float2*)&Bs[kk][tx * 2];
+                acc[0][0] += av.x * bv.x; acc[0][1] += av.x * bv.y;
+                acc[1][0] += av.y * bv.x; acc[1][1] += av.y * bv.y;
+            }
+        }
+        #pragma unroll
+        for (int u = 0; u < 2; ++u)
+            #pragma unroll
+            for (int v = 0; v < 2; ++v) {
+                int c = rowbase + ty * 2 + u, e = colbase + tx * 2 + v;
+                float a = acc[u][v];
+                unsigned short hu = f2bf_u(a);
+                size_t fidx = (((size_t)(e >> 4) * 56 + i * 8 + (c >> 5)) * 64
+                               + (e & 15) + (((c >> 3) & 3) << 4)) * 8 + (c & 7);
+                DThi[fidx] = hu;
+                DTlo[fidx] = f2bf_u(a - bfu2f(hu));
+            }
+    }
 }
 
 __global__ __launch_bounds__(256) void final_gemm_mfma_kernel(
@@ -674,24 +669,22 @@
     unsigned short* DThi = (unsigned short*)(ws + 8323072);
     unsigned short* DTlo = (unsigned short*)(ws + 8552448);
     float* d0     = ws + 8781824;
-    float* c0     = Mtmp;
-
-    conv_kernel<<<1696, 256, 0, stream>>>(query, key, value, in_proj_w,
-                                          s_l_w, s_a_w, s_v_w, out_w,
-                                          XFh, XFl, WFh, WFl,
-                                          GFh, GFl, OWFh, OWFl);
-    qkv_mfma_kernel<<<dim3(12, 192), 256, 0, stream>>>(XFh, XFl, WFh, WFl,
-                                                       in_proj_b, query, qws,
-                                                       KRh, KRl, VFh, VFl);
-    wcomb1_mfma_kernel<<<dim3(4, 16, 7), 256, 0, stream>>>(GFh, GFl, OWFh, OWFl,
-                                                           Mtmp);
-    attn_mfma_kernel<<<dim3(24, 32), 256, 0, stream>>>(qws, KRh, KRl, VFh, VFl,
-                                                       Ohi, Olo);
-    wcomb2_gemm_kernel<<<dim3(8, 8, 7), 256, 0, stream>>>(Mtmp, final_w, query,
-                                                          DThi, DTlo);
-    bias1_kernel<<<256, 256, 0, stream>>>(s_l_w, s_a_w, s_v_w, out_b,
-                                          s_l_b, s_a_b, s_v_b, query, c0);
-    bias2_kernel<<<256, 256, 0, stream>>>(c0, final_w, final_b, query, d0);
+    float* c0     = ws + 8782336;
+
+    stage1_kernel<<<1952, 256, 0, stream>>>(query, key, value, in_proj_w,
+                                            s_l_w, s_a_w, s_v_w, out_w,
+                                            out_b, s_l_b, s_a_b, s_v_b,
+                                            XFh, XFl, WFh, WFl,
+                                            GFh, GFl, OWFh, OWFl, c0);
+    stage2_kernel<<<3008, 256, 0, stream>>>(XFh, XFl, WFh, WFl,
+                                            in_proj_b, query, qws,
+                                            KRh, KRl, VFh, VFl,
+                                            GFh, GFl, OWFh, OWFl, Mtmp,
+                                            c0, final_w, final_b, d0);
+    stage3_kernel<<<1216, 256, 0, stream>>>(qws, KRh, KRl, VFh, VFl,
+                                            Ohi, Olo,
+                                            Mtmp, final_w, query,
+                                            DThi, DTlo);
     final_gemm_mfma_kernel<<<dim3(4, 192), 256, 0, stream>>>(Ohi, Olo, DThi, DTlo,
                                                              d0, query, d_out);
 }
```

Result: faster. 172.2 us (-6.1%).
